# Optimization experiments

Hardware: AMD Instinct MI355X
Metric: run time of the kernel (lower is better)

Reference implementation:

```python
import jax, jax.numpy as jnp
import numpy as np

BN_EPS = 1e-5

def _batchnorm(x, gamma, beta):
    # training-mode BN over node dim (axis 0), biased variance (torch semantics)
    mean = jnp.mean(x, axis=0)
    var = jnp.mean(jnp.square(x - mean), axis=0)
    return (x - mean) * jax.lax.rsqrt(var + BN_EPS) * gamma + beta

def setup_inputs() -> dict:
    key = jax.random.key(0)
    ks = jax.random.split(key, 12)
    N, E, Din, H, Hm, C = 50000, 1600000, 128, 1024, 256, 10
    def glorot(k, shape):
        fan_in, fan_out = shape[1], shape[0]
        lim = float(np.sqrt(6.0 / (fan_in + fan_out)))
        return jax.random.uniform(k, shape, jnp.float32, -lim, lim)
    return {
        "x": jax.random.normal(ks[0], (N, Din), jnp.float32),
        "edge_index": jax.random.randint(ks[1], (2, E), 0, N, jnp.int64),
        "edge_weight": jax.random.uniform(ks[2], (E,), jnp.float32),
        # ChebConv K=1: single linear W0 + bias
        "W1": glorot(ks[3], (H, Din)), "b1": jnp.zeros((H,), jnp.float32),
        "g1": jnp.ones((H,), jnp.float32), "be1": jnp.zeros((H,), jnp.float32),
        "W2": glorot(ks[4], (H, H)), "b2": jnp.zeros((H,), jnp.float32),
        "g2": jnp.ones((H,), jnp.float32), "be2": jnp.zeros((H,), jnp.float32),
        "Wl1": glorot(ks[5], (Hm, H)), "bl1": jnp.zeros((Hm,), jnp.float32),
        "Wl2": glorot(ks[6], (C, Hm)), "bl2": jnp.zeros((C,), jnp.float32),
    }

def reference(x, edge_index, edge_weight, W1, b1, g1, be1, W2, b2, g2, be2, Wl1, bl1, Wl2, bl2):
    # ChebConv(K=1) == linear on T0 term (identity); edges unused in the math.
    h = x @ W1.T + b1                       # [N, 1024]
    h = jax.nn.relu(_batchnorm(h, g1, be1))
    h = h @ W2.T + b2                       # [N, 1024]
    h = jax.nn.relu(_batchnorm(h, g2, be2))
    h = jax.nn.relu(h @ Wl1.T + bl1)        # [N, 256]
    logits = h @ Wl2.T + bl2                # [N, C]
    return jax.nn.log_softmax(logits, axis=1)
```

## Files before the change

### kernel.cpp

```cpp
#include <hip/hip_runtime.h>
#include <stdint.h>

#define BM 256
#define BN 128
#define BKK 64

typedef __attribute__((ext_vector_type(8))) __bf16 bf16x8;
typedef __attribute__((ext_vector_type(4))) float f32x4;

__device__ __forceinline__ unsigned short f2bf(float f) {
  unsigned u = __builtin_bit_cast(unsigned, f);
  u = (u + 0x7FFFu + ((u >> 16) & 1u)) >> 16;
  return (unsigned short)u;
}
__device__ __forceinline__ float bf2f(unsigned short h) {
  return __builtin_bit_cast(float, (unsigned)h << 16);
}

__device__ __forceinline__ void gld_lds16(const void* g, void* l) {
  __builtin_amdgcn_global_load_lds(
      (const __attribute__((address_space(1))) void*)g,
      (__attribute__((address_space(3))) void*)l,
      16, 0, 0);
}

__global__ void k_f32_to_bf16(const float* __restrict__ in,
                              unsigned short* __restrict__ out, int n4) {
  int i = blockIdx.x * blockDim.x + threadIdx.x;
  if (i >= n4) return;
  float4 v = ((const float4*)in)[i];
  ushort4 o;
  o.x = f2bf(v.x); o.y = f2bf(v.y); o.z = f2bf(v.z); o.w = f2bf(v.w);
  ((ushort4*)out)[i] = o;
}

template <bool STATS, bool RELU>
__global__ __launch_bounds__(256, 2) void k_gemm_bt(
    const unsigned short* __restrict__ A, const unsigned short* __restrict__ B,
    const float* __restrict__ bias, unsigned short* __restrict__ C,
    float* __restrict__ sum, float* __restrict__ sumsq,
    int M, int N, int K) {
  __shared__ alignas(16) unsigned short As[BM * BKK];
  __shared__ alignas(16) unsigned short Bs[BN * BKK];

  const int gx = gridDim.x;
  const int nwg = gx * gridDim.y;
  const int flat = blockIdx.x + gx * blockIdx.y;
  const int q = nwg >> 3, r = nwg & 7;
  const int xcd = flat & 7, idx = flat >> 3;
  const int g = (xcd < r ? xcd * (q + 1) : r * (q + 1) + (xcd - r) * q) + idx;
  const int row0 = (g / gx) * BM;
  const int col0 = (g % gx) * BN;

  const int tid = threadIdx.x;
  const int lane = tid & 63;
  const int w = tid >> 6;
  const int wr = w >> 1, wc = w & 1;
  const int l15 = lane & 15, l4 = lane >> 4;

  const int c_swz = (((lane & 7) ^ (lane >> 3)) * 8);

  f32x4 acc[8][4];
#pragma unroll
  for (int i = 0; i < 8; ++i)
#pragma unroll
    for (int j = 0; j < 4; ++j) acc[i][j] = f32x4{0.f, 0.f, 0.f, 0.f};

  for (int k0 = 0; k0 < K; k0 += BKK) {
#pragma unroll
    for (int i = 0; i < 8; ++i) {
      const int e = i * 2048 + w * 512 + lane * 8;
      const int rr = e >> 6;
      int ar = row0 + rr;
      ar = ar < M ? ar : M - 1;
      gld_lds16(A + (size_t)ar * K + k0 + c_swz, As + i * 2048 + w * 512);
    }
#pragma unroll
    for (int i = 0; i < 4; ++i) {
      const int e = i * 2048 + w * 512 + lane * 8;
      const int rr = e >> 6;
      gld_lds16(B + (size_t)(col0 + rr) * K + k0 + c_swz, Bs + i * 2048 + w * 512);
    }
    __syncthreads();
#pragma unroll
    for (int kk = 0; kk < 2; ++kk) {
      const int cs = (((kk * 4 + l4) ^ (l15 & 7)) * 8);
      bf16x8 a[8], b[4];
#pragma unroll
      for (int mi = 0; mi < 8; ++mi)
        a[mi] = *(const bf16x8*)(As + (wr * 128 + mi * 16 + l15) * BKK + cs);
#pragma unroll
      for (int ni = 0; ni < 4; ++ni)
        b[ni] = *(const bf16x8*)(Bs + (wc * 64 + ni * 16 + l15) * BKK + cs);
#pragma unroll
      for (int mi = 0; mi < 8; ++mi)
#pragma unroll
        for (int ni = 0; ni < 4; ++ni)
          acc[mi][ni] = __builtin_amdgcn_mfma_f32_16x16x32_bf16(a[mi], b[ni], acc[mi][ni], 0, 0, 0);
    }
    __syncthreads();
  }

  float s[4] = {0.f, 0.f, 0.f, 0.f}, qs[4] = {0.f, 0.f, 0.f, 0.f};
#pragma unroll
  for (int mi = 0; mi < 8; ++mi) {
    const int rbase = row0 + wr * 128 + mi * 16 + l4 * 4;
#pragma unroll
    for (int ni = 0; ni < 4; ++ni) {
      const int col = col0 + wc * 64 + ni * 16 + l15;
      const float bv = bias[col];
#pragma unroll
      for (int rr = 0; rr < 4; ++rr) {
        const int row = rbase + rr;
        if (row < M) {
          float v = acc[mi][ni][rr] + bv;
          if (RELU) v = fmaxf(v, 0.f);
          C[(size_t)row * N + col] = f2bf(v);
          if (STATS) { s[ni] += v; qs[ni] += v * v; }
        }
      }
    }
  }
  if (STATS) {
#pragma unroll
    for (int ni = 0; ni < 4; ++ni) {
      s[ni] += __shfl_xor(s[ni], 16, 64);
      s[ni] += __shfl_xor(s[ni], 32, 64);
      qs[ni] += __shfl_xor(qs[ni], 16, 64);
      qs[ni] += __shfl_xor(qs[ni], 32, 64);
    }
    if (l4 == 0) {
#pragma unroll
      for (int ni = 0; ni < 4; ++ni) {
        const int col = col0 + wc * 64 + ni * 16 + l15;
        atomicAdd(&sum[col], s[ni]);
        atomicAdd(&sumsq[col], qs[ni]);
      }
    }
  }
}

__global__ void k_bn_finalize(const float* __restrict__ sum, const float* __restrict__ sumsq,
                              const float* __restrict__ g, const float* __restrict__ be,
                              float* __restrict__ scale, float* __restrict__ shift,
                              int M, int N) {
  int c = blockIdx.x * blockDim.x + threadIdx.x;
  if (c >= N) return;
  float inv = 1.f / (float)M;
  float mean = sum[c] * inv;
  float var = sumsq[c] * inv - mean * mean;
  float sc = g[c] * rsqrtf(var + 1e-5f);
  scale[c] = sc;
  shift[c] = be[c] - mean * sc;
}

__global__ void k_bn_apply(unsigned short* __restrict__ Hb,
                           const float* __restrict__ scale,
                           const float* __restrict__ shift, size_t total8) {
  size_t i = (size_t)blockIdx.x * blockDim.x + threadIdx.x;
  if (i >= total8) return;
  size_t b = i * 8;
  uint4 v = *(uint4*)(Hb + b);
  const int c = (int)(b & 1023);
  const float4 sc0 = *(const float4*)(scale + c);
  const float4 sc1 = *(const float4*)(scale + c + 4);
  const float4 sh0 = *(const float4*)(shift + c);
  const float4 sh1 = *(const float4*)(shift + c + 4);
  auto nrm = [](unsigned u, float scl, float sfh) -> unsigned {
    return (unsigned)f2bf(fmaxf(fmaf(bf2f((unsigned short)u), scl, sfh), 0.f));
  };
  uint4 o;
  o.x = nrm(v.x & 0xFFFF, sc0.x, sh0.x) | (nrm(v.x >> 16, sc0.y, sh0.y) << 16);
  o.y = nrm(v.y & 0xFFFF, sc0.z, sh0.z) | (nrm(v.y >> 16, sc0.w, sh0.w) << 16);
  o.z = nrm(v.z & 0xFFFF, sc1.x, sh1.x) | (nrm(v.z >> 16, sc1.y, sh1.y) << 16);
  o.w = nrm(v.w & 0xFFFF, sc1.z, sh1.z) | (nrm(v.w >> 16, sc1.w, sh1.w) << 16);
  *(uint4*)(Hb + b) = o;
}

__global__ __launch_bounds__(256) void k_head(const unsigned short* __restrict__ H3,
                                              const float* __restrict__ W,
                                              const float* __restrict__ bias,
                                              float* __restrict__ out, int M) {
  __shared__ float Ws[10 * 256];
  for (int i = threadIdx.x; i < 2560; i += 256) Ws[i] = W[i];
  __syncthreads();
  const int wv = threadIdx.x >> 6;
  const int lane = threadIdx.x & 63;
  const int row = blockIdx.x * 4 + wv;
  if (row >= M) return;
  const ushort4 hv = *(const ushort4*)(H3 + (size_t)row * 256 + lane * 4);
  const float h0 = bf2f(hv.x), h1 = bf2f(hv.y), h2 = bf2f(hv.z), h3 = bf2f(hv.w);
  float acc[10];
#pragma unroll
  for (int o = 0; o < 10; ++o) {
    const float* wp = Ws + o * 256 + lane * 4;
    acc[o] = h0 * wp[0] + h1 * wp[1] + h2 * wp[2] + h3 * wp[3];
  }
#pragma unroll
  for (int d = 1; d < 64; d <<= 1)
#pragma unroll
    for (int o = 0; o < 10; ++o) acc[o] += __shfl_xor(acc[o], d, 64);
  if (lane == 0) {
    float lg[10], mx = -1e30f;
#pragma unroll
    for (int o = 0; o < 10; ++o) {
      lg[o] = acc[o] + bias[o];
      mx = fmaxf(mx, lg[o]);
    }
    float ssum = 0.f;
#pragma unroll
    for (int o = 0; o < 10; ++o) ssum += expf(lg[o] - mx);
    float ls = logf(ssum);
#pragma unroll
    for (int o = 0; o < 10; ++o) out[(size_t)row * 10 + o] = lg[o] - mx - ls;
  }
}

extern "C" void kernel_launch(void* const* d_in, const int* in_sizes, int n_in,
                              void* d_out, int out_size, void* d_ws, size_t ws_size,
                              hipStream_t stream) {
  const float* x = (const float*)d_in[0];
  const float* W1 = (const float*)d_in[3];
  const float* b1 = (const float*)d_in[4];
  const float* g1 = (const float*)d_in[5];
  const float* be1 = (const float*)d_in[6];
  const float* W2 = (const float*)d_in[7];
  const float* b2 = (const float*)d_in[8];
  const float* g2 = (const float*)d_in[9];
  const float* be2 = (const float*)d_in[10];
  const float* Wl1 = (const float*)d_in[11];
  const float* bl1 = (const float*)d_in[12];
  const float* Wl2 = (const float*)d_in[13];
  const float* bl2 = (const float*)d_in[14];

  const int Din = 128, H = 1024, Hm = 256;
  const int M = in_sizes[0] / Din;

  char* ws = (char*)d_ws;
  size_t off = 0;
  auto alloc = [&](size_t b) -> void* {
    void* p = ws + off;
    off += (b + 255) & ~(size_t)255;
    return p;
  };

  float* sum1 = (float*)alloc(H * 4);
  float* sumsq1 = (float*)alloc(H * 4);
  float* sum2 = (float*)alloc(H * 4);
  float* sumsq2 = (float*)alloc(H * 4);
  float* scale1 = (float*)alloc(H * 4);
  float* shift1 = (float*)alloc(H * 4);
  float* scale2 = (float*)alloc(H * 4);
  float* shift2 = (float*)alloc(H * 4);
  unsigned short* W1b = (unsigned short*)alloc((size_t)H * Din * 2);
  unsigned short* W2b = (unsigned short*)alloc((size_t)H * H * 2);
  unsigned short* Wl1b = (unsigned short*)alloc((size_t)Hm * H * 2);
  unsigned short* h1 = (unsigned short*)alloc((size_t)M * H * 2);
  unsigned short* h2 = (unsigned short*)alloc((size_t)M * H * 2);
  unsigned short* xb = h2;
  unsigned short* h3 = h1;

  hipMemsetAsync(sum1, 0, (size_t)H * 4 * 4, stream);

  int n4;
  n4 = M * Din / 4;
  k_f32_to_bf16<<<(n4 + 255) / 256, 256, 0, stream>>>(x, xb, n4);
  n4 = H * Din / 4;
  k_f32_to_bf16<<<(n4 + 255) / 256, 256, 0, stream>>>(W1, W1b, n4);
  n4 = H * H / 4;
  k_f32_to_bf16<<<(n4 + 255) / 256, 256, 0, stream>>>(W2, W2b, n4);
  n4 = Hm * H / 4;
  k_f32_to_bf16<<<(n4 + 255) / 256, 256, 0, stream>>>(Wl1, Wl1b, n4);

  const int MT = (M + BM - 1) / BM;
  dim3 blk(256);
  const size_t total8 = (size_t)M * H / 8;
  const int apblk = (int)((total8 + 255) / 256);

  k_gemm_bt<true, false><<<dim3(H / BN, MT), blk, 0, stream>>>(
      xb, W1b, b1, h1, sum1, sumsq1, M, H, Din);
  k_bn_finalize<<<H / 256, 256, 0, stream>>>(sum1, sumsq1, g1, be1, scale1, shift1, M, H);
  k_bn_apply<<<apblk, 256, 0, stream>>>(h1, scale1, shift1, total8);

  k_gemm_bt<true, false><<<dim3(H / BN, MT), blk, 0, stream>>>(
      h1, W2b, b2, h2, sum2, sumsq2, M, H, H);
  k_bn_finalize<<<H / 256, 256, 0, stream>>>(sum2, sumsq2, g2, be2, scale2, shift2, M, H);
  k_bn_apply<<<apblk, 256, 0, stream>>>(h2, scale2, shift2, total8);

  k_gemm_bt<false, true><<<dim3(Hm / BN, MT), blk, 0, stream>>>(
      h2, Wl1b, bl1, h3, nullptr, nullptr, M, Hm, H);

  k_head<<<(M + 3) / 4, 256, 0, stream>>>(h3, Wl2, bl2, (float*)d_out, M);
}
```

Before: 485.3 us.

## Fuse batchnorm apply and ReLU into next GEMM's A-fragment loads

Removes the standalone BN-apply kernels and instead applies scale/shift plus ReLU to A fragments after they are read from LDS in the following GEMM. This eliminates two full read-modify-write passes over the large hidden activation tensors. In exchange, the normalization is recomputed redundantly for every column tile, adding VALU work and register pressure inside the MFMA loop.

```diff
diff --git a/kernel.cpp b/kernel.cpp
--- a/kernel.cpp
+++ b/kernel.cpp
@@ -6,6 +6,7 @@
 #define BKK 64
 
 typedef __attribute__((ext_vector_type(8))) __bf16 bf16x8;
+typedef __attribute__((ext_vector_type(8))) unsigned short u16x8;
 typedef __attribute__((ext_vector_type(4))) float f32x4;
 
 __device__ __forceinline__ unsigned short f2bf(float f) {
@@ -15,6 +16,21 @@
 }
 __device__ __forceinline__ float bf2f(unsigned short h) {
   return __builtin_bit_cast(float, (unsigned)h << 16);
+}
+
+__device__ __forceinline__ bf16x8 bnfrag(bf16x8 v, float4 s0, float4 s1,
+                                         float4 h0, float4 h1) {
+  u16x8 u = __builtin_bit_cast(u16x8, v);
+  u16x8 o;
+  o[0] = f2bf(fmaxf(fmaf(bf2f(u[0]), s0.x, h0.x), 0.f));
+  o[1] = f2bf(fmaxf(fmaf(bf2f(u[1]), s0.y, h0.y), 0.f));
+  o[2] = f2bf(fmaxf(fmaf(bf2f(u[2]), s0.z, h0.z), 0.f));
+  o[3] = f2bf(fmaxf(fmaf(bf2f(u[3]), s0.w, h0.w), 0.f));
+  o[4] = f2bf(fmaxf(fmaf(bf2f(u[4]), s1.x, h1.x), 0.f));
+  o[5] = f2bf(fmaxf(fmaf(bf2f(u[5]), s1.y, h1.y), 0.f));
+  o[6] = f2bf(fmaxf(fmaf(bf2f(u[6]), s1.z, h1.z), 0.f));
+  o[7] = f2bf(fmaxf(fmaf(bf2f(u[7]), s1.w, h1.w), 0.f));
+  return __builtin_bit_cast(bf16x8, o);
 }
 
 __device__ __forceinline__ void gld_lds16(const void* g, void* l) {
@@ -34,11 +50,12 @@
   ((ushort4*)out)[i] = o;
 }
 
-template <bool STATS, bool RELU>
+template <bool STATS, bool RELU, bool FUSEBN>
 __global__ __launch_bounds__(256, 2) void k_gemm_bt(
     const unsigned short* __restrict__ A, const unsigned short* __restrict__ B,
     const float* __restrict__ bias, unsigned short* __restrict__ C,
     float* __restrict__ sum, float* __restrict__ sumsq,
+    const float* __restrict__ bnsc, const float* __restrict__ bnsh,
     int M, int N, int K) {
   __shared__ alignas(16) unsigned short As[BM * BKK];
   __shared__ alignas(16) unsigned short Bs[BN * BKK];
@@ -84,6 +101,14 @@
     __syncthreads();
 #pragma unroll
     for (int kk = 0; kk < 2; ++kk) {
+      float4 s0, s1, h0, h1;
+      if (FUSEBN) {
+        const int kc = k0 + (kk * 4 + l4) * 8;
+        s0 = *(const float4*)(bnsc + kc);
+        s1 = *(const float4*)(bnsc + kc + 4);
+        h0 = *(const float4*)(bnsh + kc);
+        h1 = *(const float4*)(bnsh + kc + 4);
+      }
       const int cs = (((kk * 4 + l4) ^ (l15 & 7)) * 8);
       bf16x8 a[8], b[4];
 #pragma unroll
@@ -92,6 +117,10 @@
 #pragma unroll
       for (int ni = 0; ni < 4; ++ni)
         b[ni] = *(const bf16x8*)(Bs + (wc * 64 + ni * 16 + l15) * BKK + cs);
+      if (FUSEBN) {
+#pragma unroll
+        for (int mi = 0; mi < 8; ++mi) a[mi] = bnfrag(a[mi], s0, s1, h0, h1);
+      }
 #pragma unroll
       for (int mi = 0; mi < 8; ++mi)
 #pragma unroll
@@ -152,29 +181,6 @@
   float sc = g[c] * rsqrtf(var + 1e-5f);
   scale[c] = sc;
   shift[c] = be[c] - mean * sc;
-}
-
-__global__ void k_bn_apply(unsigned short* __restrict__ Hb,
-                           const float* __restrict__ scale,
-                           const float* __restrict__ shift, size_t total8) {
-  size_t i = (size_t)blockIdx.x * blockDim.x + threadIdx.x;
-  if (i >= total8) return;
-  size_t b = i * 8;
-  uint4 v = *(uint4*)(Hb + b);
-  const int c = (int)(b & 1023);
-  const float4 sc0 = *(const float4*)(scale + c);
-  const float4 sc1 = *(const float4*)(scale + c + 4);
-  const float4 sh0 = *(const float4*)(shift + c);
-  const float4 sh1 = *(const float4*)(shift + c + 4);
-  auto nrm = [](unsigned u, float scl, float sfh) -> unsigned {
-    return (unsigned)f2bf(fmaxf(fmaf(bf2f((unsigned short)u), scl, sfh), 0.f));
-  };
-  uint4 o;
-  o.x = nrm(v.x & 0xFFFF, sc0.x, sh0.x) | (nrm(v.x >> 16, sc0.y, sh0.y) << 16);
-  o.y = nrm(v.y & 0xFFFF, sc0.z, sh0.z) | (nrm(v.y >> 16, sc0.w, sh0.w) << 16);
-  o.z = nrm(v.z & 0xFFFF, sc1.x, sh1.x) | (nrm(v.z >> 16, sc1.y, sh1.y) << 16);
-  o.w = nrm(v.w & 0xFFFF, sc1.z, sh1.z) | (nrm(v.w >> 16, sc1.w, sh1.w) << 16);
-  *(uint4*)(Hb + b) = o;
 }
 
 __global__ __launch_bounds__(256) void k_head(const unsigned short* __restrict__ H3,
@@ -274,21 +280,17 @@
 
   const int MT = (M + BM - 1) / BM;
   dim3 blk(256);
-  const size_t total8 = (size_t)M * H / 8;
-  const int apblk = (int)((total8 + 255) / 256);
-
-  k_gemm_bt<true, false><<<dim3(H / BN, MT), blk, 0, stream>>>(
-      xb, W1b, b1, h1, sum1, sumsq1, M, H, Din);
+
+  k_gemm_bt<true, false, false><<<dim3(H / BN, MT), blk, 0, stream>>>(
+      xb, W1b, b1, h1, sum1, sumsq1, nullptr, nullptr, M, H, Din);
   k_bn_finalize<<<H / 256, 256, 0, stream>>>(sum1, sumsq1, g1, be1, scale1, shift1, M, H);
-  k_bn_apply<<<apblk, 256, 0, stream>>>(h1, scale1, shift1, total8);
-
-  k_gemm_bt<true, false><<<dim3(H / BN, MT), blk, 0, stream>>>(
-      h1, W2b, b2, h2, sum2, sumsq2, M, H, H);
+
+  k_gemm_bt<true, false, true><<<dim3(H / BN, MT), blk, 0, stream>>>(
+      h1, W2b, b2, h2, sum2, sumsq2, scale1, shift1, M, H, H);
   k_bn_finalize<<<H / 256, 256, 0, stream>>>(sum2, sumsq2, g2, be2, scale2, shift2, M, H);
-  k_bn_apply<<<apblk, 256, 0, stream>>>(h2, scale2, shift2, total8);
-
-  k_gemm_bt<false, true><<<dim3(Hm / BN, MT), blk, 0, stream>>>(
-      h2, Wl1b, bl1, h3, nullptr, nullptr, M, Hm, H);
+
+  k_gemm_bt<false, true, true><<<dim3(Hm / BN, MT), blk, 0, stream>>>(
+      h2, Wl1b, bl1, h3, nullptr, nullptr, scale2, shift2, M, Hm, H);
 
   k_head<<<(M + 3) / 4, 256, 0, stream>>>(h3, Wl2, bl2, (float*)d_out, M);
 }
```

After: 579.9 us. +19.5%, slower.

## Double-buffer LDS tiles to overlap global loads with MFMA compute

Applied to the files above, without the earlier changes.

Splits the GEMM main loop into stage and compute phases over two LDS buffers, prefetching the next K tile with global_load_lds while MFMAs run on the current one. Partial vmcnt waits and raw s_barrier calls replace the two __syncthreads per iteration. LDS use doubles to 96KB, so launch bounds drop to one workgroup per CU, giving up occupancy in exchange for explicit software pipelining.

```diff
diff --git a/kernel.cpp b/kernel.cpp
--- a/kernel.cpp
+++ b/kernel.cpp
@@ -35,13 +35,13 @@
 }
 
 template <bool STATS, bool RELU>
-__global__ __launch_bounds__(256, 2) void k_gemm_bt(
+__global__ __launch_bounds__(256, 1) void k_gemm_bt(
     const unsigned short* __restrict__ A, const unsigned short* __restrict__ B,
     const float* __restrict__ bias, unsigned short* __restrict__ C,
     float* __restrict__ sum, float* __restrict__ sumsq,
     int M, int N, int K) {
-  __shared__ alignas(16) unsigned short As[BM * BKK];
-  __shared__ alignas(16) unsigned short Bs[BN * BKK];
+  __shared__ alignas(16) unsigned short As[2][BM * BKK];
+  __shared__ alignas(16) unsigned short Bs[2][BN * BKK];
 
   const int gx = gridDim.x;
   const int nwg = gx * gridDim.y;
@@ -66,40 +66,58 @@
 #pragma unroll
     for (int j = 0; j < 4; ++j) acc[i][j] = f32x4{0.f, 0.f, 0.f, 0.f};
 
-  for (int k0 = 0; k0 < K; k0 += BKK) {
+  auto stage = [&](int buf, int k0) {
 #pragma unroll
     for (int i = 0; i < 8; ++i) {
       const int e = i * 2048 + w * 512 + lane * 8;
       const int rr = e >> 6;
       int ar = row0 + rr;
       ar = ar < M ? ar : M - 1;
-      gld_lds16(A + (size_t)ar * K + k0 + c_swz, As + i * 2048 + w * 512);
+      gld_lds16(A + (size_t)ar * K + k0 + c_swz, &As[buf][i * 2048 + w * 512]);
     }
 #pragma unroll
     for (int i = 0; i < 4; ++i) {
       const int e = i * 2048 + w * 512 + lane * 8;
       const int rr = e >> 6;
-      gld_lds16(B + (size_t)(col0 + rr) * K + k0 + c_swz, Bs + i * 2048 + w * 512);
-    }
-    __syncthreads();
+      gld_lds16(B + (size_t)(col0 + rr) * K + k0 + c_swz, &Bs[buf][i * 2048 + w * 512]);
+    }
+  };
+  auto compute = [&](int buf) {
 #pragma unroll
     for (int kk = 0; kk < 2; ++kk) {
       const int cs = (((kk * 4 + l4) ^ (l15 & 7)) * 8);
       bf16x8 a[8], b[4];
 #pragma unroll
       for (int mi = 0; mi < 8; ++mi)
-        a[mi] = *(const bf16x8*)(As + (wr * 128 + mi * 16 + l15) * BKK + cs);
+        a[mi] = *(const bf16x8*)(&As[buf][(wr * 128 + mi * 16 + l15) * BKK + cs]);
 #pragma unroll
       for (int ni = 0; ni < 4; ++ni)
-        b[ni] = *(const bf16x8*)(Bs + (wc * 64 + ni * 16 + l15) * BKK + cs);
+        b[ni] = *(const bf16x8*)(&Bs[buf][(wc * 64 + ni * 16 + l15) * BKK + cs]);
 #pragma unroll
       for (int mi = 0; mi < 8; ++mi)
 #pragma unroll
         for (int ni = 0; ni < 4; ++ni)
           acc[mi][ni] = __builtin_amdgcn_mfma_f32_16x16x32_bf16(a[mi], b[ni], acc[mi][ni], 0, 0, 0);
     }
-    __syncthreads();
-  }
+  };
+
+  const int nt = K / BKK;
+  stage(0, 0);
+  int cur = 0;
+  for (int t = 0; t < nt - 1; ++t) {
+    stage(cur ^ 1, (t + 1) * BKK);
+    asm volatile("s_waitcnt vmcnt(12)" ::: "memory");
+    __builtin_amdgcn_s_barrier();
+    __builtin_amdgcn_sched_barrier(0);
+    compute(cur);
+    __builtin_amdgcn_sched_barrier(0);
+    __builtin_amdgcn_s_barrier();
+    cur ^= 1;
+  }
+  asm volatile("s_waitcnt vmcnt(0)" ::: "memory");
+  __builtin_amdgcn_s_barrier();
+  __builtin_amdgcn_sched_barrier(0);
+  compute(cur);
 
   float s[4] = {0.f, 0.f, 0.f, 0.f}, qs[4] = {0.f, 0.f, 0.f, 0.f};
 #pragma unroll
```

Result: slower. 677.1 us (+39.5%).
